# Kernel tuning notes

Measured on AMD Instinct MI355X. Metric: run time of the kernel, lower is better.

## Reference

```python
import jax, jax.numpy as jnp
import numpy as np

B, S, D, H, DH, L, F, V, C = 2, 4096, 768, 12, 64, 2, 3072, 50265, 256
NB = S // C
NEG = -1e9


def layer_norm(x, g, b, eps=1e-5):
    m = jnp.mean(x, -1, keepdims=True)
    v = jnp.mean((x - m) ** 2, -1, keepdims=True)
    return (x - m) * jax.lax.rsqrt(v + eps) * g + b


def _blockify(t):
    # t: [B,H,S,DH] -> [B,H,NB,3C,DH], key blocks (b-1, b, b+1) per query block
    tp = jnp.pad(t, ((0, 0), (0, 0), (C, C), (0, 0)))
    tb = tp.reshape(t.shape[0], t.shape[1], NB + 2, C, DH)
    return jnp.concatenate([tb[:, :, :-2], tb[:, :, 1:-1], tb[:, :, 2:]], axis=3)


def sw_attention(x, mask, Wq, bq, Wk, bk, Wv, bv, Wo, bo):
    Bq = x.shape[0]
    def heads(w, b):
        return (x @ w + b).reshape(Bq, S, H, DH).transpose(0, 2, 1, 3)
    q = heads(Wq, bq) / jnp.sqrt(jnp.float32(DH))
    k = heads(Wk, bk)
    v = heads(Wv, bv)
    qb = q.reshape(Bq, H, NB, C, DH)
    k3, v3 = _blockify(k), _blockify(v)
    scores = jnp.einsum('bhncd,bhnkd->bhnck', qb, k3)  # [B,H,NB,C,3C]
    cc = jnp.arange(C)[:, None]
    kk = jnp.arange(3 * C)[None, :]
    band = (kk >= cc) & (kk <= cc + 2 * C)  # exact |i-j| <= 256 sliding window
    lm = mask.at[:, 0].set(0.0)  # global (CLS) key handled separately, not in band
    mp = jnp.pad(lm, ((0, 0), (C, C))).reshape(Bq, NB + 2, C)
    m3 = jnp.concatenate([mp[:, :-2], mp[:, 1:-1], mp[:, 2:]], axis=2)  # [B,NB,3C]
    valid = band[None, None, None] & (m3[:, None, :, None, :] > 0)
    scores = jnp.where(valid, scores, NEG)
    gk, gv = k[:, :, 0, :], v[:, :, 0, :]  # CLS global key/value
    gsc = jnp.einsum('bhncd,bhd->bhnc', qb, gk)[..., None]  # [B,H,NB,C,1]
    gmask = (mask[:, 0] > 0).reshape(Bq, 1, 1, 1, 1)
    gsc = jnp.where(gmask, gsc, NEG)
    probs = jax.nn.softmax(jnp.concatenate([scores, gsc], -1), -1)
    ctx = (jnp.einsum('bhnck,bhnkd->bhncd', probs[..., :3 * C], v3)
           + probs[..., 3 * C:] * gv[:, :, None, None, :])
    ctx = ctx.reshape(Bq, H, S, DH)
    # CLS is a global query: full attention over all keys
    s0 = jnp.einsum('bhd,bhsd->bhs', q[:, :, 0, :], k)
    s0 = jnp.where(mask[:, None, :] > 0, s0, NEG)
    o0 = jnp.einsum('bhs,bhsd->bhd', jax.nn.softmax(s0, -1), v)
    ctx = ctx.at[:, :, 0, :].set(o0)
    out = ctx.transpose(0, 2, 1, 3).reshape(Bq, S, D)
    return out @ Wo + bo


def setup_inputs() -> dict:
    key = jax.random.key(0)
    ks = jax.random.split(key, 16)
    def w(k, shape, s=0.02):
        return (jax.random.normal(k, shape) * s).astype(jnp.float32)
    return {
        'input_ids': jax.random.randint(ks[0], (B, S), 0, V, dtype=jnp.int32),
        'attention_mask': jnp.ones((B, S), dtype=jnp.int32),
        'emb_tok': w(ks[1], (V, D)),
        'emb_pos': w(ks[2], (S, D)),
        'emb_ln_g': jnp.ones((D,), jnp.float32),
        'emb_ln_b': jnp.zeros((D,), jnp.float32),
        'Wq': w(ks[3], (L, D, D)), 'bq': jnp.zeros((L, D), jnp.float32),
        'Wk': w(ks[4], (L, D, D)), 'bk': jnp.zeros((L, D), jnp.float32),
        'Wv': w(ks[5], (L, D, D)), 'bv': jnp.zeros((L, D), jnp.float32),
        'Wo': w(ks[6], (L, D, D)), 'bo': jnp.zeros((L, D), jnp.float32),
        'ln1_g': jnp.ones((L, D), jnp.float32), 'ln1_b': jnp.zeros((L, D), jnp.float32),
        'W1': w(ks[7], (L, D, F)), 'b1': jnp.zeros((L, F), jnp.float32),
        'W2': w(ks[8], (L, F, D)), 'b2': jnp.zeros((L, D), jnp.float32),
        'ln2_g': jnp.ones((L, D), jnp.float32), 'ln2_b': jnp.zeros((L, D), jnp.float32),
        'cls_W': w(ks[9], (D, 3)), 'cls_b': jnp.zeros((3,), jnp.float32),
    }


def reference(input_ids, attention_mask, emb_tok, emb_pos, emb_ln_g, emb_ln_b,
              Wq, bq, Wk, bk, Wv, bv, Wo, bo, ln1_g, ln1_b,
              W1, b1, W2, b2, ln2_g, ln2_b, cls_W, cls_b):
    mask = attention_mask.astype(jnp.float32)
    h = layer_norm(emb_tok[input_ids] + emb_pos[None], emb_ln_g, emb_ln_b)
    for l in range(L):
        a = sw_attention(h, mask, Wq[l], bq[l], Wk[l], bk[l], Wv[l], bv[l], Wo[l], bo[l])
        h = layer_norm(h + a, ln1_g[l], ln1_b[l])
        f = jax.nn.gelu(h @ W1[l] + b1[l], approximate=False) @ W2[l] + b2[l]
        h = layer_norm(h + f, ln2_g[l], ln2_b[l])
    logits = h[:, 0] @ cls_W + cls_b  # dropout is identity at inference
    return logits
```

## Files before the change

kernel.cpp:

```cpp
#include <hip/hip_runtime.h>
#include <math.h>

#define BB 2
#define SS 4096
#define DD 768
#define HH 12
#define LL 2
#define FF 3072
#define CC 256
#define MM 8192
#define QB 128
#define QKVN 2304

using frag8 = __attribute__((ext_vector_type(8))) short;
using f32x4 = __attribute__((ext_vector_type(4))) float;

__device__ __forceinline__ unsigned short f2b(float f) {
  unsigned u = __float_as_uint(f);
  u = u + 0x7fffu + ((u >> 16) & 1u);
  return (unsigned short)(u >> 16);
}
__device__ __forceinline__ unsigned pack2(float a, float b) {
  return (unsigned)f2b(a) | ((unsigned)f2b(b) << 16);
}
__device__ __forceinline__ float b2f(unsigned short v) {
  return __uint_as_float(((unsigned)v) << 16);
}
__device__ __forceinline__ void unpack8(int4 t, float* f) {
  unsigned u;
  u = (unsigned)t.x; f[0] = __uint_as_float(u << 16); f[1] = __uint_as_float(u & 0xffff0000u);
  u = (unsigned)t.y; f[2] = __uint_as_float(u << 16); f[3] = __uint_as_float(u & 0xffff0000u);
  u = (unsigned)t.z; f[4] = __uint_as_float(u << 16); f[5] = __uint_as_float(u & 0xffff0000u);
  u = (unsigned)t.w; f[6] = __uint_as_float(u << 16); f[7] = __uint_as_float(u & 0xffff0000u);
}
__device__ __forceinline__ void reduce2(float& s1, float& s2) {
#pragma unroll
  for (int off = 32; off > 0; off >>= 1) {
    s1 += __shfl_down(s1, off);
    s2 += __shfl_down(s2, off);
  }
  __shared__ float r1[4], r2[4];
  const int lane = threadIdx.x & 63, wv = threadIdx.x >> 6;
  if (lane == 0) { r1[wv] = s1; r2[wv] = s2; }
  __syncthreads();
  s1 = r1[0] + r1[1] + r1[2] + r1[3];
  s2 = r2[0] + r2[1] + r2[2] + r2[3];
  __syncthreads();
}
__device__ __forceinline__ void async16(const unsigned short* g, unsigned short* l) {
  __builtin_amdgcn_global_load_lds((__attribute__((address_space(1))) void*)(g),
                                   (__attribute__((address_space(3))) void*)(l), 16, 0, 0);
}

__global__ __launch_bounds__(256) void transpose_bf16(const float* __restrict__ in,
                                                      unsigned short* __restrict__ out,
                                                      int K, int N) {
  __shared__ float t[32][33];
  const int n0 = blockIdx.x * 32, k0 = blockIdx.y * 32;
  const int tx = threadIdx.x, ty = threadIdx.y;
#pragma unroll
  for (int i = 0; i < 32; i += 8) t[ty + i][tx] = in[(size_t)(k0 + ty + i) * N + n0 + tx];
  __syncthreads();
#pragma unroll
  for (int i = 0; i < 32; i += 8) out[(size_t)(n0 + ty + i) * K + k0 + tx] = f2b(t[tx][ty + i]);
}

__global__ __launch_bounds__(256) void embed_ln(const int* __restrict__ ids,
                                                const float* __restrict__ etok,
                                                const float* __restrict__ epos,
                                                const float* __restrict__ g,
                                                const float* __restrict__ bb,
                                                float* __restrict__ h32,
                                                unsigned short* __restrict__ hB) {
  const int row = blockIdx.x;
  const int s = row & (SS - 1);
  const int id = ids[row];
  float x[3];
#pragma unroll
  for (int i = 0; i < 3; i++) {
    int j = threadIdx.x + i * 256;
    x[i] = etok[(size_t)id * DD + j] + epos[(size_t)s * DD + j];
  }
  float s1 = x[0] + x[1] + x[2];
  float s2 = x[0] * x[0] + x[1] * x[1] + x[2] * x[2];
  reduce2(s1, s2);
  const float mean = s1 * (1.f / 768.f);
  const float var = s2 * (1.f / 768.f) - mean * mean;
  const float rs = rsqrtf(var + 1e-5f);
#pragma unroll
  for (int i = 0; i < 3; i++) {
    int j = threadIdx.x + i * 256;
    float y = (x[i] - mean) * rs * g[j] + bb[j];
    h32[(size_t)row * DD + j] = y;
    hB[(size_t)row * DD + j] = f2b(y);
  }
}

__global__ __launch_bounds__(256) void ln_res(float* __restrict__ h32,
                                              const float* __restrict__ delta,
                                              const float* __restrict__ g,
                                              const float* __restrict__ bb,
                                              unsigned short* __restrict__ hB) {
  const int row = blockIdx.x;
  float x[3];
#pragma unroll
  for (int i = 0; i < 3; i++) {
    int j = threadIdx.x + i * 256;
    x[i] = h32[(size_t)row * DD + j] + delta[(size_t)row * DD + j];
  }
  float s1 = x[0] + x[1] + x[2];
  float s2 = x[0] * x[0] + x[1] * x[1] + x[2] * x[2];
  reduce2(s1, s2);
  const float mean = s1 * (1.f / 768.f);
  const float var = s2 * (1.f / 768.f) - mean * mean;
  const float rs = rsqrtf(var + 1e-5f);
#pragma unroll
  for (int i = 0; i < 3; i++) {
    int j = threadIdx.x + i * 256;
    float y = (x[i] - mean) * rs * g[j] + bb[j];
    h32[(size_t)row * DD + j] = y;
    hB[(size_t)row * DD + j] = f2b(y);
  }
}

template <int EPI>
__global__ __launch_bounds__(256) void gemm_nt(const unsigned short* __restrict__ A,
                                               const unsigned short* __restrict__ Bt,
                                               const float* __restrict__ bias0,
                                               const float* __restrict__ bias1,
                                               const float* __restrict__ bias2,
                                               float* __restrict__ outF,
                                               unsigned short* __restrict__ oq,
                                               int M, int N, int K) {
  __shared__ unsigned short sA[128 * 32];
  __shared__ unsigned short sB[128 * 32];
  const int tid = threadIdx.x;
  const int m0 = blockIdx.y * 128, n0 = blockIdx.x * 128;
  const int wave = tid >> 6, lane = tid & 63;
  const int wm = (wave >> 1) * 64, wn = (wave & 1) * 64;
  const int quad = lane >> 4, r16 = lane & 15;

  const int srow = wave * 32 + (lane >> 2);
  const int scol = (lane & 3) * 8;
  const unsigned short* gA0 = A + (size_t)(m0 + srow) * K + scol;
  const unsigned short* gA1 = gA0 + (size_t)16 * K;
  const unsigned short* gB0 = Bt + (size_t)(n0 + srow) * K + scol;
  const unsigned short* gB1 = gB0 + (size_t)16 * K;
  unsigned short* lA0 = &sA[(wave * 32) * 32];
  unsigned short* lA1 = &sA[(wave * 32 + 16) * 32];
  unsigned short* lB0 = &sB[(wave * 32) * 32];
  unsigned short* lB1 = &sB[(wave * 32 + 16) * 32];

  f32x4 acc[4][4];
#pragma unroll
  for (int i = 0; i < 4; i++)
#pragma unroll
    for (int j = 0; j < 4; j++) acc[i][j] = (f32x4){0.f, 0.f, 0.f, 0.f};

  const int kiters = K >> 5;
  for (int kt = 0; kt < kiters; kt++) {
    const int k0 = kt << 5;
    __syncthreads();
    async16(gA0 + k0, lA0);
    async16(gA1 + k0, lA1);
    async16(gB0 + k0, lB0);
    async16(gB1 + k0, lB1);
    __syncthreads();
    frag8 af[4], bf[4];
#pragma unroll
    for (int i = 0; i < 4; i++)
      af[i] = *reinterpret_cast<const frag8*>(&sA[(wm + i * 16 + r16) * 32 + quad * 8]);
#pragma unroll
    for (int j = 0; j < 4; j++)
      bf[j] = *reinterpret_cast<const frag8*>(&sB[(wn + j * 16 + r16) * 32 + quad * 8]);
#pragma unroll
    for (int i = 0; i < 4; i++)
#pragma unroll
      for (int j = 0; j < 4; j++)
        acc[i][j] = __builtin_amdgcn_mfma_f32_16x16x32_bf16(af[i], bf[j], acc[i][j], 0, 0, 0);
  }

  const int which = (EPI == 1) ? (n0 / 768) : 0;
  const float* bw = (EPI == 1) ? ((which == 0) ? bias0 : (which == 1) ? bias1 : bias2) : bias0;
  const float qsc = (EPI == 1 && which == 0) ? 0.125f : 1.f;
  const int cofs = which * 768;

#pragma unroll
  for (int i = 0; i < 4; i++)
#pragma unroll
    for (int j = 0; j < 4; j++)
#pragma unroll
      for (int rr = 0; rr < 4; rr++) {
        const int row = m0 + wm + i * 16 + quad * 4 + rr;
        const int col = n0 + wn + j * 16 + r16;
        if (EPI == 0) {
          outF[(size_t)row * N + col] = acc[i][j][rr] + bias0[col];
        } else if (EPI == 1) {
          float v = (acc[i][j][rr] + bw[col - cofs]) * qsc;
          oq[(size_t)row * N + col] = f2b(v);
        } else {
          float v = acc[i][j][rr] + bias0[col];
          float y = 1.5957691216f * (v + 0.044715f * v * v * v);
          float ge = v / (1.f + __expf(-y));
          oq[(size_t)row * N + col] = f2b(ge);
        }
      }
}

__global__ __launch_bounds__(256) void attn_win(const unsigned short* __restrict__ qkv,
                                                const int* __restrict__ mask,
                                                unsigned short* __restrict__ ctxB) {
  const int n = blockIdx.x, h = blockIdx.y, b = blockIdx.z;
  const int tid = threadIdx.x;
  const int wave = tid >> 6, lane = tid & 63;
  const int quad = lane >> 4, r16 = lane & 15;
  const size_t rowB = (size_t)(b * SS);

  __shared__ unsigned short sK[64 * 72];
  __shared__ unsigned short sVt[64 * 72];
  __shared__ unsigned short sP2[4][32 * 72];
  __shared__ __align__(16) int sM[64];

  const int qw0 = n * QB + wave * 32;

  frag8 qf[2][2];
#pragma unroll
  for (int mt = 0; mt < 2; mt++)
#pragma unroll
    for (int kh = 0; kh < 2; kh++) {
      int4 t = *reinterpret_cast<const int4*>(
          qkv + (rowB + qw0 + mt * 16 + r16) * QKVN + h * 64 + kh * 32 + quad * 8);
      qf[mt][kh] = *reinterpret_cast<frag8*>(&t);
    }

  f32x4 oacc[4][2];
#pragma unroll
  for (int dt = 0; dt < 4; dt++)
#pragma unroll
    for (int mt = 0; mt < 2; mt++) oacc[dt][mt] = (f32x4){0.f, 0.f, 0.f, 0.f};
  float mx[2], li[2];
#pragma unroll
  for (int mt = 0; mt < 2; mt++) { mx[mt] = -1e30f; li[mt] = 0.f; }

  const int kbase = n * QB - 256;
  for (int ch = -1; ch < 10; ch++) {
    const int kc = kbase + ch * 64;
    const bool isG = (ch < 0);
    __syncthreads();
    {
      const int key = tid >> 2, d0 = (tid & 3) * 16;
      const int kp = isG ? ((key == 0) ? 0 : -1) : kc + key;
      int4 a = make_int4(0, 0, 0, 0), c = make_int4(0, 0, 0, 0);
      if (kp >= 0 && kp < SS) {
        const unsigned short* src = qkv + (rowB + kp) * QKVN + 768 + h * 64 + d0;
        a = *reinterpret_cast<const int4*>(src);
        c = *reinterpret_cast<const int4*>(src + 8);
      }
      *reinterpret_cast<int4*>(&sK[key * 72 + d0]) = a;
      *reinterpret_cast<int4*>(&sK[key * 72 + d0 + 8]) = c;
    }
    {
      const int key = tid & 63, d0 = (tid >> 6) * 16;
      const int kp = isG ? ((key == 0) ? 0 : -1) : kc + key;
      int4 a = make_int4(0, 0, 0, 0), c = make_int4(0, 0, 0, 0);
      if (kp >= 0 && kp < SS) {
        const unsigned short* src = qkv + (rowB + kp) * QKVN + 1536 + h * 64 + d0;
        a = *reinterpret_cast<const int4*>(src);
        c = *reinterpret_cast<const int4*>(src + 8);
      }
      unsigned short e[16];
      *reinterpret_cast<int4*>(&e[0]) = a;
      *reinterpret_cast<int4*>(&e[8]) = c;
#pragma unroll
      for (int j = 0; j < 16; j++) sVt[(d0 + j) * 72 + key] = e[j];
    }
    if (tid < 64) {
      int ok;
      if (isG) ok = (tid == 0) ? mask[rowB] : 0;
      else {
        const int kp = kc + tid;
        ok = (kp >= 1 && kp < SS) ? mask[rowB + kp] : 0;
      }
      sM[tid] = ok;
    }
    __syncthreads();

    if (!isG && (kc > qw0 + 31 + 256 || kc + 63 < qw0 - 256)) continue;

    f32x4 sacc[4][2];
#pragma unroll
    for (int nt = 0; nt < 4; nt++)
#pragma unroll
      for (int mt = 0; mt < 2; mt++) sacc[nt][mt] = (f32x4){0.f, 0.f, 0.f, 0.f};
#pragma unroll
    for (int kh = 0; kh < 2; kh++) {
      frag8 kf[4];
#pragma unroll
      for (int nt = 0; nt < 4; nt++)
        kf[nt] = *reinterpret_cast<const frag8*>(&sK[(nt * 16 + r16) * 72 + kh * 32 + quad * 8]);
#pragma unroll
      for (int nt = 0; nt < 4; nt++)
#pragma unroll
        for (int mt = 0; mt < 2; mt++)
          sacc[nt][mt] = __builtin_amdgcn_mfma_f32_16x16x32_bf16(kf[nt], qf[mt][kh], sacc[nt][mt], 0, 0, 0);
    }

    int mv[4][4];
#pragma unroll
    for (int nt = 0; nt < 4; nt++) {
      int4 t = *reinterpret_cast<const int4*>(&sM[nt * 16 + quad * 4]);
      mv[nt][0] = t.x; mv[nt][1] = t.y; mv[nt][2] = t.z; mv[nt][3] = t.w;
    }

#pragma unroll
    for (int mt = 0; mt < 2; mt++) {
      const int qg = qw0 + mt * 16 + r16;
      float m_c = -1e30f;
#pragma unroll
      for (int nt = 0; nt < 4; nt++)
#pragma unroll
        for (int rr = 0; rr < 4; rr++) {
          const int kp = kc + nt * 16 + quad * 4 + rr;
          const bool valid = (mv[nt][rr] != 0) && (isG || (unsigned)(kp - qg + 256) <= 512u);
          const float s = valid ? sacc[nt][mt][rr] : -1e30f;
          sacc[nt][mt][rr] = s;
          m_c = fmaxf(m_c, s);
        }
      m_c = fmaxf(m_c, __shfl_xor(m_c, 16, 64));
      m_c = fmaxf(m_c, __shfl_xor(m_c, 32, 64));
      const float mnew = fmaxf(mx[mt], m_c);
      const float alpha = __expf(mx[mt] - mnew);
      mx[mt] = mnew;
      float s_c = 0.f;
#pragma unroll
      for (int nt = 0; nt < 4; nt++) {
        float pk[4];
#pragma unroll
        for (int rr = 0; rr < 4; rr++) {
          const float sv = sacc[nt][mt][rr];
          float p = __expf(sv - mnew);
          p = (sv > -5e29f) ? p : 0.f;
          s_c += p;
          pk[rr] = p;
        }
        uint2 w;
        w.x = pack2(pk[0], pk[1]);
        w.y = pack2(pk[2], pk[3]);
        *reinterpret_cast<uint2*>(&sP2[wave][(mt * 16 + r16) * 72 + nt * 16 + quad * 4]) = w;
      }
      s_c += __shfl_xor(s_c, 16, 64);
      s_c += __shfl_xor(s_c, 32, 64);
      li[mt] = li[mt] * alpha + s_c;
#pragma unroll
      for (int dt = 0; dt < 4; dt++)
#pragma unroll
        for (int rr = 0; rr < 4; rr++) oacc[dt][mt][rr] *= alpha;
    }

#pragma unroll
    for (int kh = 0; kh < 2; kh++) {
      frag8 vf[4], pf[2];
#pragma unroll
      for (int dt = 0; dt < 4; dt++)
        vf[dt] = *reinterpret_cast<const frag8*>(&sVt[(dt * 16 + r16) * 72 + kh * 32 + quad * 8]);
#pragma unroll
      for (int mt = 0; mt < 2; mt++)
        pf[mt] = *reinterpret_cast<const frag8*>(&sP2[wave][(mt * 16 + r16) * 72 + kh * 32 + quad * 8]);
#pragma unroll
      for (int dt = 0; dt < 4; dt++)
#pragma unroll
        for (int mt = 0; mt < 2; mt++)
          oacc[dt][mt] = __builtin_amdgcn_mfma_f32_16x16x32_bf16(vf[dt], pf[mt], oacc[dt][mt], 0, 0, 0);
    }
  }

#pragma unroll
  for (int mt = 0; mt < 2; mt++) {
    const float inv = 1.f / li[mt];
    const int qg = qw0 + mt * 16 + r16;
#pragma unroll
    for (int dt = 0; dt < 4; dt++) {
      uint2 w;
      w.x = pack2(oacc[dt][mt][0] * inv, oacc[dt][mt][1] * inv);
      w.y = pack2(oacc[dt][mt][2] * inv, oacc[dt][mt][3] * inv);
      *reinterpret_cast<uint2*>(ctxB + (rowB + qg) * DD + h * 64 + dt * 16 + quad * 4) = w;
    }
  }
}

__global__ __launch_bounds__(256) void attn_r0_part(const unsigned short* __restrict__ qkv,
                                                    const int* __restrict__ mask,
                                                    float* __restrict__ part) {
  const int ch = blockIdx.x, h = blockIdx.y, b = blockIdx.z;
  const int tid = threadIdx.x;
  const int lane = tid & 63, wave = tid >> 6;
  const size_t rowB = (size_t)(b * SS);

  __shared__ float sQ[64];
  __shared__ float wmx[4], wls[4];
  __shared__ float sPp[256];
  __shared__ float sO[4][64];
  if (tid < 8) {
    int4 t = *reinterpret_cast<const int4*>(qkv + rowB * QKVN + h * 64 + tid * 8);
    float f[8]; unpack8(t, f);
#pragma unroll
    for (int j = 0; j < 8; j++) sQ[tid * 8 + j] = f[j];
  }
  __syncthreads();

  const int key = ch * 256 + tid;
  float sc;
  {
    float s = 0.f;
    const unsigned short* kp = qkv + (rowB + key) * QKVN + 768 + h * 64;
#pragma unroll
    for (int i = 0; i < 8; i++) {
      int4 t = *reinterpret_cast<const int4*>(kp + i * 8);
      float f[8]; unpack8(t, f);
#pragma unroll
      for (int j = 0; j < 8; j++) s = fmaf(sQ[i * 8 + j], f[j], s);
    }
    sc = (mask[rowB + key] != 0) ? s : -1e9f;
  }
  float m = sc;
#pragma unroll
  for (int off = 1; off < 64; off <<= 1) m = fmaxf(m, __shfl_xor(m, off, 64));
  if (lane == 0) wmx[wave] = m;
  __syncthreads();
  const float Mx = fmaxf(fmaxf(wmx[0], wmx[1]), fmaxf(wmx[2], wmx[3]));
  const float p = __expf(sc - Mx);
  float ls = p;
#pragma unroll
  for (int off = 1; off < 64; off <<= 1) ls += __shfl_xor(ls, off, 64);
  sPp[tid] = p;
  if (lane == 0) wls[wave] = ls;
  __syncthreads();

  float acc = 0.f;
  const unsigned short* vb = qkv + (rowB + ch * 256 + wave * 64) * QKVN + 1536 + h * 64 + lane;
#pragma unroll 4
  for (int t = 0; t < 64; t++)
    acc = fmaf(sPp[wave * 64 + t], b2f(vb[(size_t)t * QKVN]), acc);
  sO[wave][lane] = acc;
  __syncthreads();
  if (tid < 64) {
    float* pp = part + ((size_t)((b * HH + h) * 16 + ch)) * 68;
    pp[tid] = sO[0][tid] + sO[1][tid] + sO[2][tid] + sO[3][tid];
    if (tid == 0) {
      pp[64] = Mx;
      pp[65] = wls[0] + wls[1] + wls[2] + wls[3];
    }
  }
}

__global__ __launch_bounds__(64) void attn_r0_comb(const float* __restrict__ part,
                                                   unsigned short* __restrict__ ctxB) {
  const int h = blockIdx.x, b = blockIdx.y;
  const int tid = threadIdx.x;
  const float* base = part + ((size_t)((b * HH + h) * 16)) * 68;
  float M = -1e30f;
#pragma unroll
  for (int c = 0; c < 16; c++) M = fmaxf(M, base[c * 68 + 64]);
  float L = 0.f, o = 0.f;
#pragma unroll
  for (int c = 0; c < 16; c++) {
    const float w = __expf(base[c * 68 + 64] - M);
    L += base[c * 68 + 65] * w;
    o = fmaf(w, base[c * 68 + tid], o);
  }
  ctxB[((size_t)(b * SS)) * DD + h * 64 + tid] = f2b(o / L);
}

__global__ __launch_bounds__(256) void cls_head(const float* __restrict__ h32,
                                                const float* __restrict__ W,
                                                const float* __restrict__ bc,
                                                float* __restrict__ out) {
  const int b = blockIdx.x;
  const float* hr = h32 + (size_t)b * SS * DD;
  float p0 = 0.f, p1 = 0.f, p2 = 0.f;
  for (int d = threadIdx.x; d < DD; d += 256) {
    const float x = hr[d];
    p0 = fmaf(x, W[d * 3 + 0], p0);
    p1 = fmaf(x, W[d * 3 + 1], p1);
    p2 = fmaf(x, W[d * 3 + 2], p2);
  }
  __shared__ float r0[256], r1[256], r2[256];
  r0[threadIdx.x] = p0; r1[threadIdx.x] = p1; r2[threadIdx.x] = p2;
  __syncthreads();
  if (threadIdx.x == 0) {
    float s0 = 0.f, s1 = 0.f, s2 = 0.f;
    for (int t = 0; t < 256; t++) { s0 += r0[t]; s1 += r1[t]; s2 += r2[t]; }
    out[b * 3 + 0] = s0 + bc[0];
    out[b * 3 + 1] = s1 + bc[1];
    out[b * 3 + 2] = s2 + bc[2];
  }
}

static const size_t OFF_WT = 0;
static const size_t OFF_H32 = 28311552;
static const size_t OFF_HB = 53477376;
static const size_t OFF_QKV = 66060288;
static const size_t OFF_CTX = 103809024;
static const size_t OFF_DELTA = 116391936;
static const size_t OFF_F1 = 141557760;
static const size_t WS_NEEDED = 191889408;

extern "C" void kernel_launch(void* const* d_in, const int* in_sizes, int n_in,
                              void* d_out, int out_size, void* d_ws, size_t ws_size,
                              hipStream_t stream) {
  (void)in_sizes; (void)n_in; (void)out_size;
  if (ws_size < WS_NEEDED) return;

  const int* ids = (const int*)d_in[0];
  const int* mask = (const int*)d_in[1];
  const float* emb_tok = (const float*)d_in[2];
  const float* emb_pos = (const float*)d_in[3];
  const float* eg = (const float*)d_in[4];
  const float* eb = (const float*)d_in[5];
  const float* Wq = (const float*)d_in[6];
  const float* bq = (const float*)d_in[7];
  const float* Wk = (const float*)d_in[8];
  const float* bk = (const float*)d_in[9];
  const float* Wv = (const float*)d_in[10];
  const float* bv = (const float*)d_in[11];
  const float* Wo = (const float*)d_in[12];
  const float* bo = (const float*)d_in[13];
  const float* ln1g = (const float*)d_in[14];
  const float* ln1b = (const float*)d_in[15];
  const float* W1 = (const float*)d_in[16];
  const float* b1 = (const float*)d_in[17];
  const float* W2 = (const float*)d_in[18];
  const float* b2 = (const float*)d_in[19];
  const float* ln2g = (const float*)d_in[20];
  const float* ln2b = (const float*)d_in[21];
  const float* clsW = (const float*)d_in[22];
  const float* clsb = (const float*)d_in[23];
  float* out = (float*)d_out;

  char* ws = (char*)d_ws;
  unsigned short* wt = (unsigned short*)(ws + OFF_WT);
  float* h32 = (float*)(ws + OFF_H32);
  unsigned short* hB = (unsigned short*)(ws + OFF_HB);
  unsigned short* qkvB = (unsigned short*)(ws + OFF_QKV);
  unsigned short* ctxB = (unsigned short*)(ws + OFF_CTX);
  float* delta = (float*)(ws + OFF_DELTA);
  unsigned short* f1B = (unsigned short*)(ws + OFF_F1);

  for (int l = 0; l < 2; l++) {
    const size_t lw = (size_t)l * 7077888;
    transpose_bf16<<<dim3(24, 24), dim3(32, 8), 0, stream>>>(Wq + (size_t)l * 589824, wt + lw + 0, 768, 768);
    transpose_bf16<<<dim3(24, 24), dim3(32, 8), 0, stream>>>(Wk + (size_t)l * 589824, wt + lw + 589824, 768, 768);
    transpose_bf16<<<dim3(24, 24), dim3(32, 8), 0, stream>>>(Wv + (size_t)l * 589824, wt + lw + 1179648, 768, 768);
    transpose_bf16<<<dim3(24, 24), dim3(32, 8), 0, stream>>>(Wo + (size_t)l * 589824, wt + lw + 1769472, 768, 768);
    transpose_bf16<<<dim3(96, 24), dim3(32, 8), 0, stream>>>(W1 + (size_t)l * 2359296, wt + lw + 2359296, 768, 3072);
    transpose_bf16<<<dim3(24, 96), dim3(32, 8), 0, stream>>>(W2 + (size_t)l * 2359296, wt + lw + 4718592, 3072, 768);
  }

  embed_ln<<<MM, 256, 0, stream>>>(ids, emb_tok, emb_pos, eg, eb, h32, hB);

  for (int l = 0; l < 2; l++) {
    const size_t lw = (size_t)l * 7077888;
    gemm_nt<1><<<dim3(18, 64), 256, 0, stream>>>(hB, wt + lw, bq + l * 768, bk + l * 768,
                                                 bv + l * 768, nullptr, qkvB,
                                                 MM, QKVN, 768);
    attn_win<<<dim3(SS / QB, 12, 2), 256, 0, stream>>>(qkvB, mask, ctxB);
    attn_r0_part<<<dim3(16, 12, 2), 256, 0, stream>>>(qkvB, mask, delta);
    attn_r0_comb<<<dim3(12, 2), 64, 0, stream>>>(delta, ctxB);
    gemm_nt<0><<<dim3(6, 64), 256, 0, stream>>>(ctxB, wt + lw + 1769472, bo + l * 768, nullptr,
                                                nullptr, delta, nullptr,
                                                MM, 768, 768);
    ln_res<<<MM, 256, 0, stream>>>(h32, delta, ln1g + l * 768, ln1b + l * 768, hB);
    gemm_nt<2><<<dim3(24, 64), 256, 0, stream>>>(hB, wt + lw + 2359296, b1 + l * 3072, nullptr,
                                                 nullptr, nullptr, f1B,
                                                 MM, 3072, 768);
    gemm_nt<0><<<dim3(6, 64), 256, 0, stream>>>(f1B, wt + lw + 4718592, b2 + l * 768, nullptr,
                                                nullptr, delta, nullptr,
                                                MM, 768, 3072);
    ln_res<<<MM, 256, 0, stream>>>(h32, delta, ln2g + l * 768, ln2b + l * 768, hB);
  }

  cls_head<<<dim3(BB), 256, 0, stream>>>(h32, clsW, clsb, out);
}
```

Measured before the change: 980.8 us.

## Split-K the N=768 GEMMs, swizzle tile order, and batch weight transposes

The two N=768 GEMMs (output projection and FFN down) now launch with a K-split of two. The second half writes partial sums into a scratch buffer that aliases the QKV workspace, and ln_res adds that buffer in before the residual layer norm. This doubles the block count for these 384-tile launches so more compute units stay busy. Block indices are also remapped into groups of eight M-tiles for L2 locality, and the twelve weight-transpose launches are merged into three batched launches. The cost is extra fp32 partial traffic and an additional read in ln_res.

New measurement: 920.0 us. -6.2%, faster.

```diff
diff --git a/kernel.cpp b/kernel.cpp
--- a/kernel.cpp
+++ b/kernel.cpp
@@ -52,10 +52,30 @@
                                    (__attribute__((address_space(3))) void*)(l), 16, 0, 0);
 }
 
-__global__ __launch_bounds__(256) void transpose_bf16(const float* __restrict__ in,
-                                                      unsigned short* __restrict__ out,
-                                                      int K, int N) {
+__global__ __launch_bounds__(256) void transpose_sq8(const float* __restrict__ Wq,
+                                                     const float* __restrict__ Wk,
+                                                     const float* __restrict__ Wv,
+                                                     const float* __restrict__ Wo,
+                                                     unsigned short* __restrict__ wt) {
   __shared__ float t[32][33];
+  const int z = blockIdx.z, l = z >> 2, w = z & 3;
+  const float* in = ((w == 0) ? Wq : (w == 1) ? Wk : (w == 2) ? Wv : Wo) + (size_t)l * 589824;
+  unsigned short* out = wt + (size_t)l * 7077888 + (size_t)w * 589824;
+  const int n0 = blockIdx.x * 32, k0 = blockIdx.y * 32;
+  const int tx = threadIdx.x, ty = threadIdx.y;
+#pragma unroll
+  for (int i = 0; i < 32; i += 8) t[ty + i][tx] = in[(size_t)(k0 + ty + i) * 768 + n0 + tx];
+  __syncthreads();
+#pragma unroll
+  for (int i = 0; i < 32; i += 8) out[(size_t)(n0 + ty + i) * 768 + k0 + tx] = f2b(t[tx][ty + i]);
+}
+
+__global__ __launch_bounds__(256) void transpose_bz(const float* __restrict__ in0,
+                                                    unsigned short* __restrict__ out0,
+                                                    int K, int N, size_t sStride, size_t dStride) {
+  __shared__ float t[32][33];
+  const float* in = in0 + (size_t)blockIdx.z * sStride;
+  unsigned short* out = out0 + (size_t)blockIdx.z * dStride;
   const int n0 = blockIdx.x * 32, k0 = blockIdx.y * 32;
   const int tx = threadIdx.x, ty = threadIdx.y;
 #pragma unroll
@@ -98,6 +118,7 @@
 
 __global__ __launch_bounds__(256) void ln_res(float* __restrict__ h32,
                                               const float* __restrict__ delta,
+                                              const float* __restrict__ delta2,
                                               const float* __restrict__ g,
                                               const float* __restrict__ bb,
                                               unsigned short* __restrict__ hB) {
@@ -107,6 +128,13 @@
   for (int i = 0; i < 3; i++) {
     int j = threadIdx.x + i * 256;
     x[i] = h32[(size_t)row * DD + j] + delta[(size_t)row * DD + j];
+  }
+  if (delta2) {
+#pragma unroll
+    for (int i = 0; i < 3; i++) {
+      int j = threadIdx.x + i * 256;
+      x[i] += delta2[(size_t)row * DD + j];
+    }
   }
   float s1 = x[0] + x[1] + x[2];
   float s2 = x[0] * x[0] + x[1] * x[1] + x[2] * x[2];
@@ -130,21 +158,31 @@
                                                const float* __restrict__ bias1,
                                                const float* __restrict__ bias2,
                                                float* __restrict__ outF,
+                                               float* __restrict__ outF2,
                                                unsigned short* __restrict__ oq,
                                                int M, int N, int K) {
   __shared__ unsigned short sA[128 * 32];
   __shared__ unsigned short sB[128 * 32];
   const int tid = threadIdx.x;
-  const int m0 = blockIdx.y * 128, n0 = blockIdx.x * 128;
+
+  const int gx = gridDim.x;
+  const int L = blockIdx.x + gx * blockIdx.y;
+  const int slot = L >> 3;
+  const int m0 = ((L & 7) + 8 * (slot / gx)) * 128;
+  const int n0 = (slot % gx) * 128;
+
+  const int kspan = K / gridDim.z;
+  const int kbeg = blockIdx.z * kspan;
+
   const int wave = tid >> 6, lane = tid & 63;
   const int wm = (wave >> 1) * 64, wn = (wave & 1) * 64;
   const int quad = lane >> 4, r16 = lane & 15;
 
   const int srow = wave * 32 + (lane >> 2);
   const int scol = (lane & 3) * 8;
-  const unsigned short* gA0 = A + (size_t)(m0 + srow) * K + scol;
+  const unsigned short* gA0 = A + (size_t)(m0 + srow) * K + kbeg + scol;
   const unsigned short* gA1 = gA0 + (size_t)16 * K;
-  const unsigned short* gB0 = Bt + (size_t)(n0 + srow) * K + scol;
+  const unsigned short* gB0 = Bt + (size_t)(n0 + srow) * K + kbeg + scol;
   const unsigned short* gB1 = gB0 + (size_t)16 * K;
   unsigned short* lA0 = &sA[(wave * 32) * 32];
   unsigned short* lA1 = &sA[(wave * 32 + 16) * 32];
@@ -157,7 +195,7 @@
 #pragma unroll
     for (int j = 0; j < 4; j++) acc[i][j] = (f32x4){0.f, 0.f, 0.f, 0.f};
 
-  const int kiters = K >> 5;
+  const int kiters = kspan >> 5;
   for (int kt = 0; kt < kiters; kt++) {
     const int k0 = kt << 5;
     __syncthreads();
@@ -185,6 +223,9 @@
   const float qsc = (EPI == 1 && which == 0) ? 0.125f : 1.f;
   const int cofs = which * 768;
 
+  float* dst = (blockIdx.z == 0) ? outF : outF2;
+  const bool addb = (blockIdx.z == 0);
+
 #pragma unroll
   for (int i = 0; i < 4; i++)
 #pragma unroll
@@ -194,7 +235,7 @@
         const int row = m0 + wm + i * 16 + quad * 4 + rr;
         const int col = n0 + wn + j * 16 + r16;
         if (EPI == 0) {
-          outF[(size_t)row * N + col] = acc[i][j][rr] + bias0[col];
+          dst[(size_t)row * N + col] = acc[i][j][rr] + (addb ? bias0[col] : 0.f);
         } else if (EPI == 1) {
           float v = (acc[i][j][rr] + bw[col - cofs]) * qsc;
           oq[(size_t)row * N + col] = f2b(v);
@@ -544,39 +585,36 @@
   unsigned short* qkvB = (unsigned short*)(ws + OFF_QKV);
   unsigned short* ctxB = (unsigned short*)(ws + OFF_CTX);
   float* delta = (float*)(ws + OFF_DELTA);
+  float* aux = (float*)(ws + OFF_QKV);
   unsigned short* f1B = (unsigned short*)(ws + OFF_F1);
 
-  for (int l = 0; l < 2; l++) {
-    const size_t lw = (size_t)l * 7077888;
-    transpose_bf16<<<dim3(24, 24), dim3(32, 8), 0, stream>>>(Wq + (size_t)l * 589824, wt + lw + 0, 768, 768);
-    transpose_bf16<<<dim3(24, 24), dim3(32, 8), 0, stream>>>(Wk + (size_t)l * 589824, wt + lw + 589824, 768, 768);
-    transpose_bf16<<<dim3(24, 24), dim3(32, 8), 0, stream>>>(Wv + (size_t)l * 589824, wt + lw + 1179648, 768, 768);
-    transpose_bf16<<<dim3(24, 24), dim3(32, 8), 0, stream>>>(Wo + (size_t)l * 589824, wt + lw + 1769472, 768, 768);
-    transpose_bf16<<<dim3(96, 24), dim3(32, 8), 0, stream>>>(W1 + (size_t)l * 2359296, wt + lw + 2359296, 768, 3072);
-    transpose_bf16<<<dim3(24, 96), dim3(32, 8), 0, stream>>>(W2 + (size_t)l * 2359296, wt + lw + 4718592, 3072, 768);
-  }
+  transpose_sq8<<<dim3(24, 24, 8), dim3(32, 8), 0, stream>>>(Wq, Wk, Wv, Wo, wt);
+  transpose_bz<<<dim3(96, 24, 2), dim3(32, 8), 0, stream>>>(W1, wt + 2359296, 768, 3072,
+                                                            2359296, 7077888);
+  transpose_bz<<<dim3(24, 96, 2), dim3(32, 8), 0, stream>>>(W2, wt + 4718592, 3072, 768,
+                                                            2359296, 7077888);
 
   embed_ln<<<MM, 256, 0, stream>>>(ids, emb_tok, emb_pos, eg, eb, h32, hB);
 
   for (int l = 0; l < 2; l++) {
     const size_t lw = (size_t)l * 7077888;
     gemm_nt<1><<<dim3(18, 64), 256, 0, stream>>>(hB, wt + lw, bq + l * 768, bk + l * 768,
-                                                 bv + l * 768, nullptr, qkvB,
+                                                 bv + l * 768, nullptr, nullptr, qkvB,
                                                  MM, QKVN, 768);
     attn_win<<<dim3(SS / QB, 12, 2), 256, 0, stream>>>(qkvB, mask, ctxB);
     attn_r0_part<<<dim3(16, 12, 2), 256, 0, stream>>>(qkvB, mask, delta);
     attn_r0_comb<<<dim3(12, 2), 64, 0, stream>>>(delta, ctxB);
-    gemm_nt<0><<<dim3(6, 64), 256, 0, stream>>>(ctxB, wt + lw + 1769472, bo + l * 768, nullptr,
-                                                nullptr, delta, nullptr,
-                                                MM, 768, 768);
-    ln_res<<<MM, 256, 0, stream>>>(h32, delta, ln1g + l * 768, ln1b + l * 768, hB);
-    gemm_nt<2><<<dim3(24, 64), 256, 0, stream>>>(hB, wt + lw + 2359296, b1 + l * 3072, nullptr,
-                                                 nullptr, nullptr, f1B,
+    gemm_nt<0><<<dim3(6, 64, 2), 256, 0, stream>>>(ctxB, wt + lw + 1769472, bo + l * 768,
+                                                   nullptr, nullptr, delta, aux, nullptr,
+                                                   MM, 768, 768);
+    ln_res<<<MM, 256, 0, stream>>>(h32, delta, aux, ln1g + l * 768, ln1b + l * 768, hB);
+    gemm_nt<2><<<dim3(24, 64), 256, 0, stream>>>(hB, wt + lw + 2359296, b1 + l * 3072,
+                                                 nullptr, nullptr, nullptr, nullptr, f1B,
                                                  MM, 3072, 768);
-    gemm_nt<0><<<dim3(6, 64), 256, 0, stream>>>(f1B, wt + lw + 4718592, b2 + l * 768, nullptr,
-                                                nullptr, delta, nullptr,
-                                                MM, 768, 3072);
-    ln_res<<<MM, 256, 0, stream>>>(h32, delta, ln2g + l * 768, ln2b + l * 768, hB);
+    gemm_nt<0><<<dim3(6, 64, 2), 256, 0, stream>>>(f1B, wt + lw + 4718592, b2 + l * 768,
+                                                   nullptr, nullptr, delta, aux, nullptr,
+                                                   MM, 768, 3072);
+    ln_res<<<MM, 256, 0, stream>>>(h32, delta, aux, ln2g + l * 768, ln2b + l * 768, hB);
   }
 
   cls_head<<<dim3(BB), 256, 0, stream>>>(h32, clsW, clsb, out);
```
